# Kernel tuning notes

Hardware: AMD Instinct MI355X
Metric: run time of the kernel (lower is better)

Reference implementation:

```python
import jax, jax.numpy as jnp
import numpy as np

N = 100000
E = 1600000
F_IN = 128
HID = 64
NUM_CLASSES = 40


def setup_inputs() -> dict:
    key = jax.random.key(0)
    ks = jax.random.split(key, 8)
    x = jax.random.normal(ks[0], (N, F_IN), dtype=jnp.float32)
    edge_index = jax.random.randint(ks[1], (2, E), 0, N, dtype=jnp.int32)
    s1 = 1.0 / np.sqrt(F_IN)
    s2 = 1.0 / np.sqrt(HID)
    W1_l = jax.random.normal(ks[2], (F_IN, HID), dtype=jnp.float32) * s1
    W1_r = jax.random.normal(ks[3], (F_IN, HID), dtype=jnp.float32) * s1
    b1 = jnp.zeros((HID,), dtype=jnp.float32)
    W2_l = jax.random.normal(ks[4], (HID, NUM_CLASSES), dtype=jnp.float32) * s2
    W2_r = jax.random.normal(ks[5], (HID, NUM_CLASSES), dtype=jnp.float32) * s2
    b2 = jnp.zeros((NUM_CLASSES,), dtype=jnp.float32)
    return {"x": x, "edge_index": edge_index, "W1_l": W1_l, "W1_r": W1_r,
            "b1": b1, "W2_l": W2_l, "W2_r": W2_r, "b2": b2}


def _mean_aggregate(x, src, dst, num_nodes):
    # gather source features along edges, scatter-mean into destinations
    summed = jax.ops.segment_sum(x[src], dst, num_segments=num_nodes)  # [N, F]
    deg = jax.ops.segment_sum(jnp.ones((src.shape[0],), x.dtype), dst,
                              num_segments=num_nodes)  # [N]
    return summed / jnp.maximum(deg, 1.0)[:, None]


def _sage_conv(x, src, dst, W_l, W_r, b):
    agg = _mean_aggregate(x, src, dst, x.shape[0])
    return agg @ W_l + x @ W_r + b


def reference(x, edge_index, W1_l, W1_r, b1, W2_l, W2_r, b2):
    src, dst = edge_index[0], edge_index[1]
    h = _sage_conv(x, src, dst, W1_l, W1_r, b1)
    h = jax.nn.relu(h)
    h = _sage_conv(h, src, dst, W2_l, W2_r, b2)
    return jax.nn.log_softmax(h, axis=1)
```

## Files before the change

kernel.cpp:

```cpp
#include <hip/hip_runtime.h>

#define F_IN 128
#define HID 64
#define NCLS 40

#define TSH 7
#define TS  128
#define NBMAX 800
#define GH 800
#define NW 256

typedef __attribute__((ext_vector_type(8))) short bf16x8;
typedef __attribute__((ext_vector_type(4))) float f32x4;
typedef __attribute__((ext_vector_type(2))) float f32x2;
typedef __attribute__((ext_vector_type(4))) int int4v;
typedef __attribute__((ext_vector_type(2))) int int2v;

__device__ __forceinline__ unsigned short f2b(float f) {
    union { float f; unsigned int u; } v; v.f = f;
    unsigned int u = v.u + 0x7FFFu + ((v.u >> 16) & 1u);
    return (unsigned short)(u >> 16);
}
__device__ __forceinline__ float b2f(unsigned short b) {
    union { unsigned int u; float f; } v; v.u = ((unsigned int)b) << 16;
    return v.f;
}

__global__ __launch_bounds__(256) void hist_kernel(
    const int* __restrict__ dst, int* __restrict__ ghist, int E, int NB)
{
    __shared__ int h[NBMAX];
    const int tid = threadIdx.x;
    for (int i = tid; i < NBMAX; i += 256) h[i] = 0;
    __syncthreads();
    int chunk = (E + NW - 1) / NW;
    chunk = (chunk + 3) & ~3;
    const int lo = blockIdx.x * chunk;
    const int hi = min(E, lo + chunk);
    for (int e = lo + tid * 4; e + 3 < hi; e += 1024) {
        int4v d4 = *(const int4v*)(dst + e);
        atomicAdd(&h[d4.x >> TSH], 1);
        atomicAdd(&h[d4.y >> TSH], 1);
        atomicAdd(&h[d4.z >> TSH], 1);
        atomicAdd(&h[d4.w >> TSH], 1);
    }
    {
        int tb = hi & ~3;
        if (tb < hi) {
            for (int e = tb + tid; e < hi; e += 256)
                atomicAdd(&h[dst[e] >> TSH], 1);
        }
    }
    __syncthreads();
    for (int bk = tid; bk < NB; bk += 256)
        ghist[blockIdx.x * GH + bk] = h[bk];
}

__global__ __launch_bounds__(256) void btot_kernel(
    const int* __restrict__ ghist, int* __restrict__ btot)
{
    __shared__ int s[256];
    const int bk = blockIdx.x, t = threadIdx.x;
    s[t] = ghist[t * GH + bk];
    __syncthreads();
    for (int off = 128; off > 0; off >>= 1) {
        if (t < off) s[t] += s[t + off];
        __syncthreads();
    }
    if (t == 0) btot[bk] = s[0];
}

__global__ __launch_bounds__(256) void bscan_kernel(
    const int* __restrict__ btot, int* __restrict__ bbase, int NB)
{
    __shared__ int sls[256];
    const int t = threadIdx.x;
    const int base = t * 4;
    int a[4];
    #pragma unroll
    for (int k = 0; k < 4; k++) a[k] = (base + k < NB) ? btot[base + k] : 0;
    a[1] += a[0]; a[2] += a[1]; a[3] += a[2];
    sls[t] = a[3];
    __syncthreads();
    for (int off = 1; off < 256; off <<= 1) {
        int v = (t >= off) ? sls[t - off] : 0;
        __syncthreads();
        sls[t] += v;
        __syncthreads();
    }
    const int prefix = sls[t] - a[3];
    #pragma unroll
    for (int k = 0; k < 4; k++) {
        int excl = prefix + (k > 0 ? a[k - 1] : 0);
        if (base + k < NB) bbase[base + k] = excl;
    }
    if (t == 255) bbase[NB] = sls[255];
}

__global__ __launch_bounds__(256) void boff_kernel(
    const int* __restrict__ ghist, const int* __restrict__ bbase,
    int* __restrict__ goff)
{
    __shared__ int s[256];
    const int bk = blockIdx.x, t = threadIdx.x;
    const int v = ghist[t * GH + bk];
    s[t] = v;
    __syncthreads();
    for (int off = 1; off < 256; off <<= 1) {
        int u = (t >= off) ? s[t - off] : 0;
        __syncthreads();
        s[t] += u;
        __syncthreads();
    }
    goff[bk * 256 + t] = bbase[bk] + s[t] - v;
}

__global__ __launch_bounds__(256) void part_kernel(
    const int* __restrict__ src, const int* __restrict__ dst,
    const int* __restrict__ goff, unsigned* __restrict__ staging, int E, int NB)
{
    __shared__ int cur[NBMAX];
    const int tid = threadIdx.x;
    const int blk = blockIdx.x;
    for (int bk = tid; bk < NB; bk += 256) cur[bk] = goff[bk * 256 + blk];
    __syncthreads();
    int chunk = (E + NW - 1) / NW;
    chunk = (chunk + 3) & ~3;
    const int lo = blk * chunk;
    const int hi = min(E, lo + chunk);
    for (int e = lo + tid * 4; e + 3 < hi; e += 1024) {
        int4v d4 = *(const int4v*)(dst + e);
        int4v s4 = *(const int4v*)(src + e);
        int d[4] = {d4.x, d4.y, d4.z, d4.w};
        int s[4] = {s4.x, s4.y, s4.z, s4.w};
        #pragma unroll
        for (int k = 0; k < 4; k++) {
            int bk = d[k] >> TSH;
            int p = atomicAdd(&cur[bk], 1);
            staging[p] = ((unsigned)(d[k] & (TS - 1)) << 17) | (unsigned)s[k];
        }
    }
    {
        int tb = hi & ~3;
        if (tb < hi) {
            for (int e = tb + tid; e < hi; e += 256) {
                int d = dst[e], s = src[e];
                int bk = d >> TSH;
                int p = atomicAdd(&cur[bk], 1);
                staging[p] = ((unsigned)(d & (TS - 1)) << 17) | (unsigned)s;
            }
        }
    }
}

__global__ __launch_bounds__(256) void build_kernel(
    const unsigned* __restrict__ staging, const int* __restrict__ bbase,
    int* __restrict__ rowptr, int* __restrict__ csr, int N)
{
    __shared__ int scnt[TS];
    __shared__ int sscan[TS];
    __shared__ int spos[TS];
    __shared__ int scur[TS];
    const int b = blockIdx.x, tid = threadIdx.x;
    if (tid < TS) { scnt[tid] = 0; scur[tid] = 0; }
    __syncthreads();
    const int seg0 = bbase[b], seg1 = bbase[b + 1];
    const int len = seg1 - seg0;
    const unsigned* st = staging + seg0;
    for (int i = tid; i < len; i += 256)
        atomicAdd(&scnt[(st[i] >> 17) & (TS - 1)], 1);
    __syncthreads();
    if (tid < TS) sscan[tid] = scnt[tid];
    __syncthreads();
    for (int off = 1; off < TS; off <<= 1) {
        int v = (tid < TS && tid >= off) ? sscan[tid - off] : 0;
        __syncthreads();
        if (tid < TS) sscan[tid] += v;
        __syncthreads();
    }
    const int node0 = b << TSH;
    if (tid < TS) {
        int excl = sscan[tid] - scnt[tid];
        spos[tid] = excl;
        int n = node0 + tid;
        if (n <= N) rowptr[n] = seg0 + excl;
    }
    __syncthreads();
    for (int i = tid; i < len; i += 256) {
        unsigned w = st[i];
        int dl = (w >> 17) & (TS - 1);
        int s = (int)(w & 0x1FFFFu);
        int p = atomicAdd(&scur[dl], 1);
        csr[seg0 + spos[dl] + p] = s;
    }
}

__global__ __launch_bounds__(256) void wprep_kernel(
    const float* __restrict__ W1l, const float* __restrict__ W1r,
    const float* __restrict__ W2l, const float* __restrict__ W2r,
    unsigned short* __restrict__ Wt, unsigned short* __restrict__ Wt2)
{
    const int gid = blockIdx.x * 256 + threadIdx.x;
    if (gid < 16384) {
        int k = gid >> 7;
        int c = gid & 127;
        float v = (c < 64) ? W1l[k * 64 + c] : W1r[k * 64 + (c - 64)];
        Wt[c * 128 + k] = f2b(v);
    } else if (gid < 24576) {
        int idx = gid - 16384;
        int c = idx >> 7;
        int k = idx & 127;
        float v = 0.f;
        if (c < NCLS) v = (k < 64) ? W2r[k * NCLS + c] : W2l[(k - 64) * NCLS + c];
        Wt2[c * 128 + k] = f2b(v);
    }
}

__global__ __launch_bounds__(256) void gemm1_kernel(
    const float* __restrict__ x, const unsigned short* __restrict__ Wt,
    const float* __restrict__ b1,
    unsigned char* __restrict__ p1f8, unsigned short* __restrict__ qb, int N)
{
    __shared__ alignas(16) unsigned short sW[128 * 136];
    const int tid = threadIdx.x;
    {
        const int4v* Wg = (const int4v*)Wt;
        #pragma unroll
        for (int i = 0; i < 8; i++) {
            int idx16 = i * 256 + tid;
            int c = idx16 >> 4;
            int k8 = idx16 & 15;
            int4v v = Wg[idx16];
            *(int4v*)&sW[c * 136 + k8 * 8] = v;
        }
    }
    __syncthreads();

    const int w = tid >> 6;
    const int lane = tid & 63;
    const int m = lane & 15;
    const int g = lane >> 4;

    const int node0 = blockIdx.x * 64;
    int arow = node0 + w * 16 + m;
    int arow_c = arow < N ? arow : 0;
    const float* xr = x + (size_t)arow_c * F_IN;

    f32x4 acc[8];
    #pragma unroll
    for (int c = 0; c < 8; c++) acc[c] = (f32x4){0.f, 0.f, 0.f, 0.f};

    #pragma unroll
    for (int ks = 0; ks < 4; ks++) {
        const int k0 = ks * 32 + g * 8;
        f32x4 xa = *(const f32x4*)(xr + k0);
        f32x4 xb = *(const f32x4*)(xr + k0 + 4);
        bf16x8 a;
        a[0] = (short)f2b(xa.x); a[1] = (short)f2b(xa.y);
        a[2] = (short)f2b(xa.z); a[3] = (short)f2b(xa.w);
        a[4] = (short)f2b(xb.x); a[5] = (short)f2b(xb.y);
        a[6] = (short)f2b(xb.z); a[7] = (short)f2b(xb.w);
        #pragma unroll
        for (int ct = 0; ct < 8; ct++) {
            bf16x8 b = *(const bf16x8*)&sW[(ct * 16 + m) * 136 + k0];
            acc[ct] = __builtin_amdgcn_mfma_f32_16x16x32_bf16(a, b, acc[ct], 0, 0, 0);
        }
    }

    float bias[4];
    #pragma unroll
    for (int ct = 4; ct < 8; ct++) bias[ct - 4] = b1[(ct - 4) * 16 + m];

    #pragma unroll
    for (int ct = 0; ct < 8; ct++) {
        const int col = ct * 16 + m;
        #pragma unroll
        for (int r = 0; r < 4; r++) {
            int nd = node0 + w * 16 + g * 4 + r;
            if (nd < N) {
                if (col < 64) {
                    float v = acc[ct][r];
                    int pk = __builtin_amdgcn_cvt_pk_fp8_f32(v, v, 0, false);
                    p1f8[(size_t)nd * HID + col] = (unsigned char)(pk & 0xff);
                } else {
                    qb[(size_t)nd * HID + (col - 64)] = f2b(acc[ct][r] + bias[ct - 4]);
                }
            }
        }
    }
}

#define ACC8(A, V)                                            \
    A[0] += __builtin_amdgcn_cvt_pk_f32_fp8((V).x, false);    \
    A[1] += __builtin_amdgcn_cvt_pk_f32_fp8((V).x, true);     \
    A[2] += __builtin_amdgcn_cvt_pk_f32_fp8((V).y, false);    \
    A[3] += __builtin_amdgcn_cvt_pk_f32_fp8((V).y, true);

__global__ __launch_bounds__(256) void agg1_kernel(
    const int* __restrict__ rowptr, const int* __restrict__ csr,
    const unsigned char* __restrict__ p1f8, const unsigned short* __restrict__ qb,
    unsigned short* __restrict__ hb, unsigned char* __restrict__ hf8, int N)
{
    const int wid = (blockIdx.x * 256 + threadIdx.x) >> 6;
    const int lane = threadIdx.x & 63;
    const int nw   = lane >> 4;
    const int slot = (lane >> 3) & 1;
    const int fg   = lane & 7;
    const int node = wid * 4 + nw;
    int beg = 0, end = 0;
    if (node < N) { beg = rowptr[node]; end = rowptr[node + 1]; }

    f32x2 a0[4], a1[4], a2[4], a3[4];
    #pragma unroll
    for (int q = 0; q < 4; q++) {
        a0[q] = (f32x2){0.f, 0.f}; a1[q] = (f32x2){0.f, 0.f};
        a2[q] = (f32x2){0.f, 0.f}; a3[q] = (f32x2){0.f, 0.f};
    }
    int j = beg + slot;
    for (; j + 6 < end; j += 8) {
        int s0 = csr[j];
        int s1 = csr[j + 2];
        int s2 = csr[j + 4];
        int s3 = csr[j + 6];
        int2v v0 = *(const int2v*)(p1f8 + (size_t)s0 * HID + fg * 8);
        int2v v1 = *(const int2v*)(p1f8 + (size_t)s1 * HID + fg * 8);
        int2v v2 = *(const int2v*)(p1f8 + (size_t)s2 * HID + fg * 8);
        int2v v3 = *(const int2v*)(p1f8 + (size_t)s3 * HID + fg * 8);
        ACC8(a0, v0) ACC8(a1, v1) ACC8(a2, v2) ACC8(a3, v3)
    }
    for (; j < end; j += 2) {
        int s0 = csr[j];
        int2v v0 = *(const int2v*)(p1f8 + (size_t)s0 * HID + fg * 8);
        ACC8(a0, v0)
    }
    float acc[8];
    #pragma unroll
    for (int q = 0; q < 4; q++) {
        acc[2 * q]     = (a0[q].x + a1[q].x) + (a2[q].x + a3[q].x);
        acc[2 * q + 1] = (a0[q].y + a1[q].y) + (a2[q].y + a3[q].y);
    }
    #pragma unroll
    for (int k = 0; k < 8; k++) acc[k] += __shfl_xor(acc[k], 8);

    if (slot == 0 && node < N) {
        float dg = (float)(end - beg);
        dg = dg > 1.f ? dg : 1.f;
        float inv = 1.f / dg;
        bf16x8 q = *(const bf16x8*)(qb + (size_t)node * HID + fg * 8);
        float hv[8];
        bf16x8 ov;
        #pragma unroll
        for (int k = 0; k < 8; k++) {
            float v = acc[k] * inv + b2f((unsigned short)q[k]);
            v = v > 0.f ? v : 0.f;
            hv[k] = v;
            ov[k] = (short)f2b(v);
        }
        *(bf16x8*)(hb + (size_t)node * HID + fg * 8) = ov;
        int w0 = __builtin_amdgcn_cvt_pk_fp8_f32(hv[0], hv[1], 0, false);
        w0     = __builtin_amdgcn_cvt_pk_fp8_f32(hv[2], hv[3], w0, true);
        int w1 = __builtin_amdgcn_cvt_pk_fp8_f32(hv[4], hv[5], 0, false);
        w1     = __builtin_amdgcn_cvt_pk_fp8_f32(hv[6], hv[7], w1, true);
        int2v wv; wv.x = w0; wv.y = w1;
        *(int2v*)(hf8 + (size_t)node * HID + fg * 8) = wv;
    }
}

__global__ __launch_bounds__(256) void agg2_kernel(
    const int* __restrict__ rowptr, const int* __restrict__ csr,
    const unsigned char* __restrict__ hf8, unsigned short* __restrict__ agghb, int N)
{
    const int wid = (blockIdx.x * 256 + threadIdx.x) >> 6;
    const int lane = threadIdx.x & 63;
    const int nw   = lane >> 4;
    const int slot = (lane >> 3) & 1;
    const int fg   = lane & 7;
    const int node = wid * 4 + nw;
    int beg = 0, end = 0;
    if (node < N) { beg = rowptr[node]; end = rowptr[node + 1]; }

    f32x2 a0[4], a1[4], a2[4], a3[4];
    #pragma unroll
    for (int q = 0; q < 4; q++) {
        a0[q] = (f32x2){0.f, 0.f}; a1[q] = (f32x2){0.f, 0.f};
        a2[q] = (f32x2){0.f, 0.f}; a3[q] = (f32x2){0.f, 0.f};
    }
    int j = beg + slot;
    for (; j + 6 < end; j += 8) {
        int s0 = csr[j];
        int s1 = csr[j + 2];
        int s2 = csr[j + 4];
        int s3 = csr[j + 6];
        int2v v0 = *(const int2v*)(hf8 + (size_t)s0 * HID + fg * 8);
        int2v v1 = *(const int2v*)(hf8 + (size_t)s1 * HID + fg * 8);
        int2v v2 = *(const int2v*)(hf8 + (size_t)s2 * HID + fg * 8);
        int2v v3 = *(const int2v*)(hf8 + (size_t)s3 * HID + fg * 8);
        ACC8(a0, v0) ACC8(a1, v1) ACC8(a2, v2) ACC8(a3, v3)
    }
    for (; j < end; j += 2) {
        int s0 = csr[j];
        int2v v0 = *(const int2v*)(hf8 + (size_t)s0 * HID + fg * 8);
        ACC8(a0, v0)
    }
    float acc[8];
    #pragma unroll
    for (int q = 0; q < 4; q++) {
        acc[2 * q]     = (a0[q].x + a1[q].x) + (a2[q].x + a3[q].x);
        acc[2 * q + 1] = (a0[q].y + a1[q].y) + (a2[q].y + a3[q].y);
    }
    #pragma unroll
    for (int k = 0; k < 8; k++) acc[k] += __shfl_xor(acc[k], 8);

    if (slot == 0 && node < N) {
        float dg = (float)(end - beg);
        dg = dg > 1.f ? dg : 1.f;
        float inv = 1.f / dg;
        bf16x8 ov;
        #pragma unroll
        for (int k = 0; k < 8; k++) ov[k] = (short)f2b(acc[k] * inv);
        *(bf16x8*)(agghb + (size_t)node * HID + fg * 8) = ov;
    }
}

__global__ __launch_bounds__(256) void final_kernel(
    const unsigned short* __restrict__ hb, const unsigned short* __restrict__ agghb,
    const unsigned short* __restrict__ Wt2, const float* __restrict__ b2,
    float* __restrict__ out, int N)
{
    __shared__ alignas(16) unsigned short sW[64 * 136];
    const int tid = threadIdx.x;
    {
        const int4v* Wg = (const int4v*)Wt2;
        #pragma unroll
        for (int i = 0; i < 4; i++) {
            int idx16 = i * 256 + tid;
            int c = idx16 >> 4;
            int k8 = idx16 & 15;
            int4v v = Wg[idx16];
            *(int4v*)&sW[c * 136 + k8 * 8] = v;
        }
    }
    __syncthreads();

    const int w = tid >> 6;
    const int lane = tid & 63;
    const int m = lane & 15;
    const int g = lane >> 4;

    const int node0 = blockIdx.x * 64;
    int arow = node0 + w * 16 + m;
    int arow_c = arow < N ? arow : 0;
    const unsigned short* hr = hb + (size_t)arow_c * HID;
    const unsigned short* ar = agghb + (size_t)arow_c * HID;

    f32x4 acc[3];
    #pragma unroll
    for (int c = 0; c < 3; c++) acc[c] = (f32x4){0.f, 0.f, 0.f, 0.f};

    #pragma unroll
    for (int ks = 0; ks < 4; ks++) {
        const int k0 = ks * 32 + g * 8;
        bf16x8 a = (k0 < 64) ? *(const bf16x8*)(hr + k0)
                             : *(const bf16x8*)(ar + (k0 - 64));
        #pragma unroll
        for (int ct = 0; ct < 3; ct++) {
            bf16x8 b = *(const bf16x8*)&sW[(ct * 16 + m) * 136 + k0];
            acc[ct] = __builtin_amdgcn_mfma_f32_16x16x32_bf16(a, b, acc[ct], 0, 0, 0);
        }
    }

    float bias[3];
    #pragma unroll
    for (int ct = 0; ct < 3; ct++) {
        int col = ct * 16 + m;
        bias[ct] = (col < NCLS) ? b2[col] : 0.f;
    }
    const bool v2 = (m < 8);

    #pragma unroll
    for (int r = 0; r < 4; r++) {
        int nd = node0 + w * 16 + g * 4 + r;
        float l0 = acc[0][r] + bias[0];
        float l1 = acc[1][r] + bias[1];
        float l2 = acc[2][r] + bias[2];
        float mx = fmaxf(l0, l1);
        if (v2) mx = fmaxf(mx, l2);
        mx = fmaxf(mx, __shfl_xor(mx, 1));
        mx = fmaxf(mx, __shfl_xor(mx, 2));
        mx = fmaxf(mx, __shfl_xor(mx, 4));
        mx = fmaxf(mx, __shfl_xor(mx, 8));
        float s = __expf(l0 - mx) + __expf(l1 - mx) + (v2 ? __expf(l2 - mx) : 0.f);
        s += __shfl_xor(s, 1);
        s += __shfl_xor(s, 2);
        s += __shfl_xor(s, 4);
        s += __shfl_xor(s, 8);
        float lse = mx + __logf(s);
        if (nd < N) {
            float* orow = out + (size_t)nd * NCLS;
            orow[m] = l0 - lse;
            orow[16 + m] = l1 - lse;
            if (v2) orow[32 + m] = l2 - lse;
        }
    }
}

extern "C" void kernel_launch(void* const* d_in, const int* in_sizes, int n_in,
                              void* d_out, int out_size, void* d_ws, size_t ws_size,
                              hipStream_t stream) {
    const float* x   = (const float*)d_in[0];
    const int*   ei  = (const int*)d_in[1];
    const float* W1l = (const float*)d_in[2];
    const float* W1r = (const float*)d_in[3];
    const float* b1  = (const float*)d_in[4];
    const float* W2l = (const float*)d_in[5];
    const float* W2r = (const float*)d_in[6];
    const float* b2  = (const float*)d_in[7];

    const int N = in_sizes[0] / F_IN;
    const int E = in_sizes[1] / 2;
    const int* src = ei;
    const int* dst = ei + E;
    const int NB = (N + TS - 1) >> TSH;

    int* wsi = (int*)d_ws;
    size_t o = 0;
    int* rowptr = wsi + o;  o += (size_t)N + 64;
    int* btot   = wsi + o;  o += 1024;
    int* bbase  = wsi + o;  o += 1024;
    int* ghist  = wsi + o;  o += (size_t)NW * GH;
    int* goff   = wsi + o;  o += (size_t)NBMAX * NW;
    o = (o + 63) & ~(size_t)63;
    unsigned* staging = (unsigned*)(wsi + o);  o += E;
    int* csr    = wsi + o;  o += E;
    o = (o + 63) & ~(size_t)63;
    unsigned short* Wt  = (unsigned short*)(wsi + o);  o += 8192;
    unsigned short* Wt2 = (unsigned short*)(wsi + o);  o += 4096;
    unsigned char*  p1f8 = (unsigned char*)(wsi + o);  o += (size_t)16 * N;
    unsigned char*  hf8  = (unsigned char*)(wsi + o);  o += (size_t)16 * N;
    unsigned short* hb   = (unsigned short*)(wsi + o); o += (size_t)32 * N;
    unsigned short* qb   = (unsigned short*)(wsi + o); o += (size_t)32 * N;
    unsigned short* agghb = qb;
    float* out  = (float*)d_out;

    hist_kernel <<<NW, 256, 0, stream>>>(dst, ghist, E, NB);
    btot_kernel <<<NB, 256, 0, stream>>>(ghist, btot);
    bscan_kernel<<<1, 256, 0, stream>>>(btot, bbase, NB);
    boff_kernel <<<NB, 256, 0, stream>>>(ghist, bbase, goff);
    part_kernel <<<NW, 256, 0, stream>>>(src, dst, goff, staging, E, NB);
    build_kernel<<<NB, 256, 0, stream>>>(staging, bbase, rowptr, csr, N);

    wprep_kernel<<<96, 256, 0, stream>>>(W1l, W1r, W2l, W2r, Wt, Wt2);
    gemm1_kernel<<<(N + 63) / 64, 256, 0, stream>>>(x, Wt, b1, p1f8, qb, N);
    agg1_kernel<<<(N + 15) / 16, 256, 0, stream>>>(rowptr, csr, p1f8, qb, hb, hf8, N);
    agg2_kernel<<<(N + 15) / 16, 256, 0, stream>>>(rowptr, csr, hf8, agghb, N);
    final_kernel<<<(N + 63) / 64, 256, 0, stream>>>(hb, agghb, Wt2, b2, out, N);
}
```

Baseline: 131.3 us.

## Fuse layer-2 mean aggregation into final GEMM kernel via shared memory

```diff
diff --git a/kernel.cpp b/kernel.cpp
--- a/kernel.cpp
+++ b/kernel.cpp
@@ -366,69 +366,17 @@
     }
 }
 
-__global__ __launch_bounds__(256) void agg2_kernel(
+__global__ __launch_bounds__(256) void final_kernel(
     const int* __restrict__ rowptr, const int* __restrict__ csr,
-    const unsigned char* __restrict__ hf8, unsigned short* __restrict__ agghb, int N)
-{
-    const int wid = (blockIdx.x * 256 + threadIdx.x) >> 6;
-    const int lane = threadIdx.x & 63;
-    const int nw   = lane >> 4;
-    const int slot = (lane >> 3) & 1;
-    const int fg   = lane & 7;
-    const int node = wid * 4 + nw;
-    int beg = 0, end = 0;
-    if (node < N) { beg = rowptr[node]; end = rowptr[node + 1]; }
-
-    f32x2 a0[4], a1[4], a2[4], a3[4];
-    #pragma unroll
-    for (int q = 0; q < 4; q++) {
-        a0[q] = (f32x2){0.f, 0.f}; a1[q] = (f32x2){0.f, 0.f};
-        a2[q] = (f32x2){0.f, 0.f}; a3[q] = (f32x2){0.f, 0.f};
-    }
-    int j = beg + slot;
-    for (; j + 6 < end; j += 8) {
-        int s0 = csr[j];
-        int s1 = csr[j + 2];
-        int s2 = csr[j + 4];
-        int s3 = csr[j + 6];
-        int2v v0 = *(const int2v*)(hf8 + (size_t)s0 * HID + fg * 8);
-        int2v v1 = *(const int2v*)(hf8 + (size_t)s1 * HID + fg * 8);
-        int2v v2 = *(const int2v*)(hf8 + (size_t)s2 * HID + fg * 8);
-        int2v v3 = *(const int2v*)(hf8 + (size_t)s3 * HID + fg * 8);
-        ACC8(a0, v0) ACC8(a1, v1) ACC8(a2, v2) ACC8(a3, v3)
-    }
-    for (; j < end; j += 2) {
-        int s0 = csr[j];
-        int2v v0 = *(const int2v*)(hf8 + (size_t)s0 * HID + fg * 8);
-        ACC8(a0, v0)
-    }
-    float acc[8];
-    #pragma unroll
-    for (int q = 0; q < 4; q++) {
-        acc[2 * q]     = (a0[q].x + a1[q].x) + (a2[q].x + a3[q].x);
-        acc[2 * q + 1] = (a0[q].y + a1[q].y) + (a2[q].y + a3[q].y);
-    }
-    #pragma unroll
-    for (int k = 0; k < 8; k++) acc[k] += __shfl_xor(acc[k], 8);
-
-    if (slot == 0 && node < N) {
-        float dg = (float)(end - beg);
-        dg = dg > 1.f ? dg : 1.f;
-        float inv = 1.f / dg;
-        bf16x8 ov;
-        #pragma unroll
-        for (int k = 0; k < 8; k++) ov[k] = (short)f2b(acc[k] * inv);
-        *(bf16x8*)(agghb + (size_t)node * HID + fg * 8) = ov;
-    }
-}
-
-__global__ __launch_bounds__(256) void final_kernel(
-    const unsigned short* __restrict__ hb, const unsigned short* __restrict__ agghb,
+    const unsigned char* __restrict__ hf8,
+    const unsigned short* __restrict__ hb,
     const unsigned short* __restrict__ Wt2, const float* __restrict__ b2,
     float* __restrict__ out, int N)
 {
     __shared__ alignas(16) unsigned short sW[64 * 136];
+    __shared__ alignas(16) unsigned short sagg[64 * 72];
     const int tid = threadIdx.x;
+    const int node0 = blockIdx.x * 64;
     {
         const int4v* Wg = (const int4v*)Wt2;
         #pragma unroll
@@ -440,18 +388,79 @@
             *(int4v*)&sW[c * 136 + k8 * 8] = v;
         }
     }
+    {
+        int4v z = (int4v){0, 0, 0, 0};
+        #pragma unroll
+        for (int i = 0; i < 3; i++) {
+            int idx16 = i * 256 + tid;
+            if (idx16 < 576) *(int4v*)&sagg[idx16 * 8] = z;
+        }
+    }
     __syncthreads();
 
     const int w = tid >> 6;
     const int lane = tid & 63;
+
+    {
+        const int nw   = lane >> 4;
+        const int slot = (lane >> 3) & 1;
+        const int fg   = lane & 7;
+        #pragma unroll
+        for (int rd = 0; rd < 4; rd++) {
+            const int nloc = w * 16 + rd * 4 + nw;
+            const int node = node0 + nloc;
+            int beg = 0, end = 0;
+            if (node < N) { beg = rowptr[node]; end = rowptr[node + 1]; }
+            f32x2 a0[4], a1[4], a2[4], a3[4];
+            #pragma unroll
+            for (int q = 0; q < 4; q++) {
+                a0[q] = (f32x2){0.f, 0.f}; a1[q] = (f32x2){0.f, 0.f};
+                a2[q] = (f32x2){0.f, 0.f}; a3[q] = (f32x2){0.f, 0.f};
+            }
+            int j = beg + slot;
+            for (; j + 6 < end; j += 8) {
+                int s0 = csr[j];
+                int s1 = csr[j + 2];
+                int s2 = csr[j + 4];
+                int s3 = csr[j + 6];
+                int2v v0 = *(const int2v*)(hf8 + (size_t)s0 * HID + fg * 8);
+                int2v v1 = *(const int2v*)(hf8 + (size_t)s1 * HID + fg * 8);
+                int2v v2 = *(const int2v*)(hf8 + (size_t)s2 * HID + fg * 8);
+                int2v v3 = *(const int2v*)(hf8 + (size_t)s3 * HID + fg * 8);
+                ACC8(a0, v0) ACC8(a1, v1) ACC8(a2, v2) ACC8(a3, v3)
+            }
+            for (; j < end; j += 2) {
+                int s0 = csr[j];
+                int2v v0 = *(const int2v*)(hf8 + (size_t)s0 * HID + fg * 8);
+                ACC8(a0, v0)
+            }
+            float acc[8];
+            #pragma unroll
+            for (int q = 0; q < 4; q++) {
+                acc[2 * q]     = (a0[q].x + a1[q].x) + (a2[q].x + a3[q].x);
+                acc[2 * q + 1] = (a0[q].y + a1[q].y) + (a2[q].y + a3[q].y);
+            }
+            #pragma unroll
+            for (int k = 0; k < 8; k++) acc[k] += __shfl_xor(acc[k], 8);
+            if (slot == 0 && node < N) {
+                float dg = (float)(end - beg);
+                dg = dg > 1.f ? dg : 1.f;
+                float inv = 1.f / dg;
+                bf16x8 ov;
+                #pragma unroll
+                for (int k = 0; k < 8; k++) ov[k] = (short)f2b(acc[k] * inv);
+                *(bf16x8*)&sagg[nloc * 72 + fg * 8] = ov;
+            }
+        }
+    }
+    __syncthreads();
+
     const int m = lane & 15;
     const int g = lane >> 4;
-
-    const int node0 = blockIdx.x * 64;
     int arow = node0 + w * 16 + m;
     int arow_c = arow < N ? arow : 0;
     const unsigned short* hr = hb + (size_t)arow_c * HID;
-    const unsigned short* ar = agghb + (size_t)arow_c * HID;
+    const unsigned short* sr = &sagg[(w * 16 + m) * 72];
 
     f32x4 acc[3];
     #pragma unroll
@@ -461,7 +470,7 @@
     for (int ks = 0; ks < 4; ks++) {
         const int k0 = ks * 32 + g * 8;
         bf16x8 a = (k0 < 64) ? *(const bf16x8*)(hr + k0)
-                             : *(const bf16x8*)(ar + (k0 - 64));
+                             : *(const bf16x8*)(sr + (k0 - 64));
         #pragma unroll
         for (int ct = 0; ct < 3; ct++) {
             bf16x8 b = *(const bf16x8*)&sW[(ct * 16 + m) * 136 + k0];
@@ -539,7 +548,6 @@
     unsigned char*  hf8  = (unsigned char*)(wsi + o);  o += (size_t)16 * N;
     unsigned short* hb   = (unsigned short*)(wsi + o); o += (size_t)32 * N;
     unsigned short* qb   = (unsigned short*)(wsi + o); o += (size_t)32 * N;
-    unsigned short* agghb = qb;
     float* out  = (float*)d_out;
 
     hist_kernel <<<NW, 256, 0, stream>>>(dst, ghist, E, NB);
@@ -552,6 +560,5 @@
     wprep_kernel<<<96, 256, 0, stream>>>(W1l, W1r, W2l, W2r, Wt, Wt2);
     gemm1_kernel<<<(N + 63) / 64, 256, 0, stream>>>(x, Wt, b1, p1f8, qb, N);
     agg1_kernel<<<(N + 15) / 16, 256, 0, stream>>>(rowptr, csr, p1f8, qb, hb, hf8, N);
-    agg2_kernel<<<(N + 15) / 16, 256, 0, stream>>>(rowptr, csr, hf8, agghb, N);
-    final_kernel<<<(N + 63) / 64, 256, 0, stream>>>(hb, agghb, Wt2, b2, out, N);
-}
+    final_kernel<<<(N + 63) / 64, 256, 0, stream>>>(rowptr, csr, hf8, hb, Wt2, b2, out, N);
+}
```

After: 138.6 us. +5.6%, slower.
